# Kernel optimization log

Hardware: AMD Instinct MI355X
Metric: run time of the kernel (lower is better)

Reference implementation:

```python
import jax, jax.numpy as jnp
import numpy as np

B, T, V, E, H, C = 128, 512, 100000, 100, 128, 3


def _lstm_dir(xs, w_ih, w_hh, b, reverse=False):
    # xs: [T,B,D]; w_ih: [4H,D]; w_hh: [4H,H]; b: [4H] (b_ih+b_hh combined)
    Tn, Bn, _ = xs.shape
    Hn = w_hh.shape[1]
    if reverse:
        xs = xs[::-1]
    gx = jnp.einsum('tbd,gd->tbg', xs, w_ih) + b  # [T,B,4H] input projections

    def step(carry, g_in):
        h, c = carry
        gates = g_in + h @ w_hh.T
        i, f, g, o = jnp.split(gates, 4, axis=-1)  # torch gate order i,f,g,o
        i = jax.nn.sigmoid(i)
        f = jax.nn.sigmoid(f)
        g = jnp.tanh(g)
        o = jax.nn.sigmoid(o)
        c = f * c + i * g
        h = o * jnp.tanh(c)
        return (h, c), h

    init = (jnp.zeros((Bn, Hn), xs.dtype), jnp.zeros((Bn, Hn), xs.dtype))
    (h_last, _), hs = jax.lax.scan(step, init, gx)
    if reverse:
        hs = hs[::-1]
    return hs, h_last


def setup_inputs() -> dict:
    key = jax.random.key(0)
    ks = jax.random.split(key, 24)
    s_e = 1.0 / np.sqrt(H)

    def u(k, shape):
        return jax.random.uniform(k, shape, jnp.float32, -s_e, s_e)

    x = jax.random.randint(ks[0], (B, T), 0, V, dtype=jnp.int32)
    emb = jax.random.normal(ks[1], (V, E), jnp.float32)
    emb = emb.at[0].set(0.0)  # padding_idx=0
    inp = {'x': x, 'emb': emb}
    names = []
    idx = 2
    for layer, din in ((0, E), (1, 2 * H)):
        for suf in ('', 'r'):
            inp[f'w_ih_l{layer}{suf}'] = u(ks[idx], (4 * H, din)); idx += 1
            inp[f'w_hh_l{layer}{suf}'] = u(ks[idx], (4 * H, H)); idx += 1
            inp[f'b_ih_l{layer}{suf}'] = u(ks[idx], (4 * H,)); idx += 1
            inp[f'b_hh_l{layer}{suf}'] = u(ks[idx], (4 * H,)); idx += 1
    s_f = 1.0 / np.sqrt(2 * H)
    inp['fc_w'] = jax.random.uniform(ks[22], (C, 2 * H), jnp.float32, -s_f, s_f)
    inp['fc_b'] = jax.random.uniform(ks[23], (C,), jnp.float32, -s_f, s_f)
    return inp


def reference(x, emb, w_ih_l0, w_hh_l0, b_ih_l0, b_hh_l0,
              w_ih_l0r, w_hh_l0r, b_ih_l0r, b_hh_l0r,
              w_ih_l1, w_hh_l1, b_ih_l1, b_hh_l1,
              w_ih_l1r, w_hh_l1r, b_ih_l1r, b_hh_l1r,
              fc_w, fc_b):
    # dropout is identity in eval mode
    xe = emb[x]                      # [B,T,E]
    xs = jnp.transpose(xe, (1, 0, 2))  # [T,B,E]
    # layer 0 bidirectional
    hf0, _ = _lstm_dir(xs, w_ih_l0, w_hh_l0, b_ih_l0 + b_hh_l0, reverse=False)
    hb0, _ = _lstm_dir(xs, w_ih_l0r, w_hh_l0r, b_ih_l0r + b_hh_l0r, reverse=True)
    x1 = jnp.concatenate([hf0, hb0], axis=-1)  # [T,B,2H]
    # layer 1 bidirectional; only final hidden states needed
    _, hF = _lstm_dir(x1, w_ih_l1, w_hh_l1, b_ih_l1 + b_hh_l1, reverse=False)
    _, hB = _lstm_dir(x1, w_ih_l1r, w_hh_l1r, b_ih_l1r + b_hh_l1r, reverse=True)
    out = jnp.concatenate([hF, hB], axis=1)  # [B,2H] == cat(hidden[-2], hidden[-1])
    return out @ fc_w.T + fc_b  # [B,C]
```

## Files before the change

kernel.cpp:

```cpp
#include <hip/hip_runtime.h>
#include <hip/hip_bf16.h>
#include <math.h>

#define TT 512
#define BB 128
#define EE 100
#define HH 128
#define G4 512
#define K1 256

typedef __attribute__((ext_vector_type(8))) short bf16x8;
typedef __attribute__((ext_vector_type(4))) float f32x4;

__device__ inline unsigned short bf16_rne(float v) {
    __hip_bfloat16 h = __float2bfloat16(v);
    return *reinterpret_cast<unsigned short*>(&h);
}

__device__ inline void gload16(const void* g, void* l) {
    __builtin_amdgcn_global_load_lds(
        (const __attribute__((address_space(1))) void*)g,
        (__attribute__((address_space(3))) void*)l, 16, 0, 0);
}

template<int CTRL>
__device__ inline float dppf(float x) {
    int r = __builtin_amdgcn_update_dpp(0, __float_as_int(x), CTRL, 0xF, 0xF, true);
    return __int_as_float(r);
}

__global__ void embed_cvt(const int* __restrict__ x, const float* __restrict__ emb,
                          unsigned short* __restrict__ xs2) {
    int row = blockIdx.x;
    int k = threadIdx.x;
    int b = row & 127, t = row >> 7;
    int tok = x[b * TT + t];
    float v = (k < EE) ? emb[(size_t)tok * EE + k] : 0.f;
    xs2[(size_t)row * 128 + k] = bf16_rne(v);
}

__global__ void wcvt2(const float* __restrict__ srcf, const float* __restrict__ srcr,
                      int Kin, int Kp,
                      unsigned short* __restrict__ dstf, unsigned short* __restrict__ dstr) {
    const float* src = blockIdx.y ? srcr : srcf;
    unsigned short* dst = blockIdx.y ? dstr : dstf;
    int n = blockIdx.x;
    int k = threadIdx.x;
    int j = n & 3;
    int gate = ((j & 1) << 1) | (j >> 1);
    int r = gate * 128 + (n >> 2);
    float v = (k < Kin) ? src[(size_t)r * Kin + k] : 0.f;
    dst[(size_t)n * Kp + k] = bf16_rne(v);
}

__global__ void bias2(const float* __restrict__ bihf0, const float* __restrict__ bhhf0,
                      const float* __restrict__ bihr0, const float* __restrict__ bhhr0,
                      const float* __restrict__ bihf1, const float* __restrict__ bhhf1,
                      const float* __restrict__ bihr1, const float* __restrict__ bhhr1,
                      float* __restrict__ dst) {
    int n = blockIdx.x * 256 + threadIdx.x;
    int layer = n >> 10;
    int d = (n >> 9) & 1, m = n & 511;
    int j = m & 3;
    int gate = ((j & 1) << 1) | (j >> 1);
    int src = gate * 128 + (m >> 2);
    const float* a = layer ? (d ? bihr1 : bihf1) : (d ? bihr0 : bihf0);
    const float* c = layer ? (d ? bhhr1 : bhhf1) : (d ? bhhr0 : bhhf0);
    dst[n] = a[src] + c[src];
}

__global__ void whh_pack4(const float* __restrict__ w0f, const float* __restrict__ w0r,
                          const float* __restrict__ w1f, const float* __restrict__ w1r,
                          float* __restrict__ dstbase) {
    int which = blockIdx.y;
    const float* src = which == 0 ? w0f : which == 1 ? w0r : which == 2 ? w1f : w1r;
    float* dst = dstbase + (size_t)which * 128 * 128 * 4;
    int u = blockIdx.x;
    int k = threadIdx.x;
    float4 v;
    v.x = src[((size_t)(0 * 128 + u)) * 128 + k];
    v.y = src[((size_t)(1 * 128 + u)) * 128 + k];
    v.z = src[((size_t)(2 * 128 + u)) * 128 + k];
    v.w = src[((size_t)(3 * 128 + u)) * 128 + k];
    reinterpret_cast<float4*>(dst)[(size_t)u * 128 + k] = v;
}

template<int K2>
__global__ __launch_bounds__(256) void gemm_mfma(
    const unsigned short* __restrict__ A2,
    const unsigned short* __restrict__ W2cat,
    const float* __restrict__ biascat,
    float* __restrict__ Cf, float* __restrict__ Cr,
    int t_base)
{
    __shared__ bf16x8 As[1024];
    __shared__ bf16x8 Bs[1024];
    int tid = threadIdx.x;
    int s = blockIdx.y;
    int dir = blockIdx.x >> 2;
    int nBase = (blockIdx.x & 3) * 128;
    int t = dir ? (TT - 1 - t_base - s) : (t_base + s);
    float* C = dir ? Cr : Cf;
    const unsigned short* Abase = A2 + (size_t)t * BB * K2;
    const unsigned short* Wbase = W2cat + (size_t)(dir * 512 + nBase) * K2;
    int lane = tid & 63, wid = tid >> 6;
    int wr = wid >> 1, wc = wid & 1;
    int l15 = lane & 15, g = lane >> 4;

    f32x4 acc[4][4];
    const f32x4 z = {0.f, 0.f, 0.f, 0.f};
    #pragma unroll
    for (int i = 0; i < 4; ++i)
        #pragma unroll
        for (int j = 0; j < 4; ++j) acc[i][j] = z;

    for (int kt = 0; kt < K2 / 64; ++kt) {
        #pragma unroll
        for (int j = 0; j < 4; ++j) {
            int p = tid + j * 256;
            int row = p >> 3;
            int k16 = (p & 7) ^ (row & 7);
            size_t goff = (size_t)row * K2 + kt * 64 + k16 * 8;
            gload16(Abase + goff, &As[p]);
            gload16(Wbase + goff, &Bs[p]);
        }
        __syncthreads();
        #pragma unroll
        for (int ks = 0; ks < 2; ++ks) {
            bf16x8 af[4], bfr[4];
            #pragma unroll
            for (int i = 0; i < 4; ++i) {
                int arow = wr * 64 + i * 16 + l15;
                int abyte = arow * 128 + ((ks * 64 + g * 16) ^ ((arow & 7) << 4));
                af[i] = As[abyte >> 4];
                int brow = wc * 64 + i * 16 + l15;
                int bbyte = brow * 128 + ((ks * 64 + g * 16) ^ ((brow & 7) << 4));
                bfr[i] = Bs[bbyte >> 4];
            }
            #pragma unroll
            for (int i = 0; i < 4; ++i)
                #pragma unroll
                for (int j = 0; j < 4; ++j)
                    acc[i][j] = __builtin_amdgcn_mfma_f32_16x16x32_bf16(
                        af[i], bfr[j], acc[i][j], 0, 0, 0);
        }
        __syncthreads();
    }
    int l3 = l15 & 3;
    int cquad = l15 & 12;
    bool lb0 = (l15 & 1) != 0;
    bool lb1 = (l15 & 2) != 0;
    #pragma unroll
    for (int i = 0; i < 4; ++i) {
        int row = s * 128 + wr * 64 + i * 16 + g * 4 + l3;
        float* Crow = C + (size_t)row * G4;
        #pragma unroll
        for (int j = 0; j < 4; ++j) {
            int colb = nBase + wc * 64 + j * 16 + cquad;
            float4 bv = *reinterpret_cast<const float4*>(&biascat[dir * 512 + colb]);
            f32x4 v = acc[i][j];
            float t0 = dppf<0xB1>(v[1]);
            float t1 = dppf<0xB1>(v[0]);
            float t2 = dppf<0xB1>(v[3]);
            float t3 = dppf<0xB1>(v[2]);
            float T0 = lb0 ? t0 : v[0];
            float T1 = lb0 ? v[1] : t1;
            float T2 = lb0 ? t2 : v[2];
            float T3 = lb0 ? v[3] : t3;
            float s0 = dppf<0x4E>(T2);
            float s1 = dppf<0x4E>(T3);
            float s2 = dppf<0x4E>(T0);
            float s3 = dppf<0x4E>(T1);
            float W0 = lb1 ? s0 : T0;
            float W1 = lb1 ? s1 : T1;
            float W2 = lb1 ? T2 : s2;
            float W3 = lb1 ? T3 : s3;
            float4 outv = {W0 + bv.x, W1 + bv.y, W2 + bv.z, W3 + bv.w};
            *reinterpret_cast<float4*>(&Crow[colb]) = outv;
        }
    }
}

__device__ inline float sig_fast(float z) {
    return __builtin_amdgcn_rcpf(1.f + __expf(-z));
}

__global__ __launch_bounds__(512, 2) void lstm_chunk(
    const float* __restrict__ gxf,
    const float* __restrict__ gxr,
    const float* __restrict__ wpkf,
    const float* __restrict__ wpkr,
    float* __restrict__ h_state,
    float* __restrict__ c_state,
    unsigned short* __restrict__ out_x1,
    int t_base, int TC, int init)
{
    int blk = blockIdx.x;
    int dir = blk >> 7;
    int b   = blk & 127;
    const float* gx  = dir ? gxr : gxf;
    const float* wpk = dir ? wpkr : wpkf;
    int tid = threadIdx.x;
    int u = tid >> 2, q = tid & 3;

    const f32x4* wp4 = reinterpret_cast<const f32x4*>(wpk) + ((size_t)u * 128 + q * 32);
#define LW(i) const f32x4 w##i = wp4[i];
    LW(0)  LW(1)  LW(2)  LW(3)  LW(4)  LW(5)  LW(6)  LW(7)
    LW(8)  LW(9)  LW(10) LW(11) LW(12) LW(13) LW(14) LW(15)
    LW(16) LW(17) LW(18) LW(19) LW(20) LW(21) LW(22) LW(23)
    LW(24) LW(25) LW(26) LW(27) LW(28) LW(29) LW(30) LW(31)
#undef LW

    __shared__ float hb[2][160];
    int sbase = (dir * BB + b) * HH;
    int hslot = (u >> 5) * 40 + (u & 31);
    float c = init ? 0.f : c_state[sbase + u];
    float h = init ? 0.f : h_state[sbase + u];
    if (q == 0) hb[0][hslot] = h;
    __syncthreads();

    const float* gxrow = gx + b * G4 + tid;
    float gin = gxrow[0];
    bool odd2 = (q & 2) != 0;
    float fq = (q == 1) ? 2.f : 1.f;
    float bq = (q == 1) ? -1.f : 0.f;

    for (int s = 0; s < TC; ++s) {
        int p = s & 1;
        int sn = (s + 1 < TC) ? s + 1 : s;
        float gin_next = gxrow[(size_t)sn * BB * G4];

        const float4* hb4 = reinterpret_cast<const float4*>(&hb[p][40 * q]);
        float4 hv0 = hb4[0], hv1 = hb4[1], hv2 = hb4[2], hv3 = hb4[3];
        float4 hv4 = hb4[4], hv5 = hb4[5], hv6 = hb4[6], hv7 = hb4[7];

        f32x4 a0 = {0.f,0.f,0.f,0.f}, a1 = {0.f,0.f,0.f,0.f};
        f32x4 a2 = {0.f,0.f,0.f,0.f}, a3 = {0.f,0.f,0.f,0.f};
#define FM(i0,i1,i2,i3,HV) { \
        f32x4 hh; \
        hh = f32x4{HV.x,HV.x,HV.x,HV.x}; a0 = __builtin_elementwise_fma(w##i0, hh, a0); \
        hh = f32x4{HV.y,HV.y,HV.y,HV.y}; a1 = __builtin_elementwise_fma(w##i1, hh, a1); \
        hh = f32x4{HV.z,HV.z,HV.z,HV.z}; a2 = __builtin_elementwise_fma(w##i2, hh, a2); \
        hh = f32x4{HV.w,HV.w,HV.w,HV.w}; a3 = __builtin_elementwise_fma(w##i3, hh, a3); }
        FM(0,1,2,3,hv0)    FM(4,5,6,7,hv1)    FM(8,9,10,11,hv2)  FM(12,13,14,15,hv3)
        FM(16,17,18,19,hv4) FM(20,21,22,23,hv5) FM(24,25,26,27,hv6) FM(28,29,30,31,hv7)
#undef FM
        f32x4 acc = (a0 + a1) + (a2 + a3);

        float xs = acc.x + dppf<0xB1>(acc.x);
        float ys = acc.y + dppf<0xB1>(acc.y);
        float zs = acc.z + dppf<0xB1>(acc.z);
        float ws = acc.w + dppf<0xB1>(acc.w);
        bool oddq = (q & 1) != 0;
        float sa = oddq ? zs : xs;
        float sb = oddq ? ws : ys;
        float sa2 = sa + dppf<0x4E>(sa);
        float sb2 = sb + dppf<0x4E>(sb);
        float pre_dot = odd2 ? sb2 : sa2;

        float pre = pre_dot + gin;
        float act = __builtin_fmaf(sig_fast(pre * fq), fq, bq);

        float ig = dppf<0x00>(act);
        float gg = dppf<0x55>(act);
        float fg = dppf<0xAA>(act);
        float og = dppf<0xFF>(act);

        c = fg * c + ig * gg;
        float th = __builtin_fmaf(2.f, sig_fast(2.f * c), -1.f);
        h = og * th;

        if (q == 0) {
            hb[p ^ 1][hslot] = h;
            if (out_x1) {
                int tg = dir ? (TT - 1 - (t_base + s)) : (t_base + s);
                out_x1[((size_t)tg * BB + b) * 256 + dir * HH + u] = bf16_rne(h);
            }
        }
        asm volatile("s_waitcnt lgkmcnt(0)" ::: "memory");
        __builtin_amdgcn_s_barrier();
        asm volatile("" ::: "memory");
        gin = gin_next;
    }
    if (q == 0) {
        h_state[sbase + u] = h;
        c_state[sbase + u] = c;
    }
}

__global__ void fc_kernel(const float* __restrict__ h_state,
                          const float* __restrict__ fc_w,
                          const float* __restrict__ fc_b,
                          float* __restrict__ out) {
    int tid = blockIdx.x * blockDim.x + threadIdx.x;
    if (tid >= BB * 3) return;
    int b = tid / 3;
    int c = tid % 3;
    float acc = 0.f;
    for (int j = 0; j < 256; ++j) {
        float v = (j < HH) ? h_state[((size_t)0 * BB + b) * HH + j]
                           : h_state[((size_t)1 * BB + b) * HH + (j - HH)];
        acc += v * fc_w[c * 256 + j];
    }
    out[b * 3 + c] = acc + fc_b[c];
}

extern "C" void kernel_launch(void* const* d_in, const int* in_sizes, int n_in,
                              void* d_out, int out_size, void* d_ws, size_t ws_size,
                              hipStream_t stream) {
    const int*   x        = (const int*)  d_in[0];
    const float* emb      = (const float*)d_in[1];
    const float* w_ih_l0  = (const float*)d_in[2];
    const float* w_hh_l0  = (const float*)d_in[3];
    const float* b_ih_l0  = (const float*)d_in[4];
    const float* b_hh_l0  = (const float*)d_in[5];
    const float* w_ih_l0r = (const float*)d_in[6];
    const float* w_hh_l0r = (const float*)d_in[7];
    const float* b_ih_l0r = (const float*)d_in[8];
    const float* b_hh_l0r = (const float*)d_in[9];
    const float* w_ih_l1  = (const float*)d_in[10];
    const float* w_hh_l1  = (const float*)d_in[11];
    const float* b_ih_l1  = (const float*)d_in[12];
    const float* b_hh_l1  = (const float*)d_in[13];
    const float* w_ih_l1r = (const float*)d_in[14];
    const float* w_hh_l1r = (const float*)d_in[15];
    const float* b_ih_l1r = (const float*)d_in[16];
    const float* b_hh_l1r = (const float*)d_in[17];
    const float* fc_w     = (const float*)d_in[18];
    const float* fc_b     = (const float*)d_in[19];
    float* out = (float*)d_out;
    (void)in_sizes; (void)n_in; (void)out_size;

    size_t xs2_b   = (size_t)TT * BB * 128 * 2;
    size_t x1_b    = (size_t)TT * BB * 256 * 2;
    size_t w2l0_b  = (size_t)512 * 128 * 2;
    size_t w2l1_b  = (size_t)512 * 256 * 2;
    size_t bias_b  = (size_t)1024 * 4;
    size_t wpk_b   = (size_t)128 * 128 * 4 * 4;
    size_t state_b = (size_t)2 * BB * HH * 4;
    size_t fixed = xs2_b + x1_b + 2 * w2l0_b + 2 * w2l1_b + 2 * bias_b
                 + 4 * wpk_b + 2 * state_b + 4096;
    int TC = 512;
    while (TC > 8) {
        size_t chunk2 = (size_t)TC * BB * G4 * 4 * 2;
        if (fixed + chunk2 <= ws_size) break;
        TC >>= 1;
    }
    char* ws = (char*)d_ws;
    size_t off = 0;
    unsigned short* xs2   = (unsigned short*)(ws + off); off += xs2_b;
    unsigned short* x1_2  = (unsigned short*)(ws + off); off += x1_b;
    unsigned short* w2l0f = (unsigned short*)(ws + off); off += w2l0_b;
    unsigned short* w2l0r = (unsigned short*)(ws + off); off += w2l0_b;
    unsigned short* w2l1f = (unsigned short*)(ws + off); off += w2l1_b;
    unsigned short* w2l1r = (unsigned short*)(ws + off); off += w2l1_b;
    float* biasl0  = (float*)(ws + off); off += bias_b;
    float* biasl1  = (float*)(ws + off); off += bias_b;
    float* wpk0f   = (float*)(ws + off); off += wpk_b;
    float* wpk0r   = (float*)(ws + off); off += wpk_b;
    float* wpk1f   = (float*)(ws + off); off += wpk_b;
    float* wpk1r   = (float*)(ws + off); off += wpk_b;
    float* h_state = (float*)(ws + off); off += state_b;
    float* c_state = (float*)(ws + off); off += state_b;
    float* gxf     = (float*)(ws + off); off += (size_t)TC * BB * G4 * 4;
    float* gxr     = (float*)(ws + off);

    int NC = TT / TC;
    dim3 ggrid(8, TC);

    embed_cvt<<<TT * BB, 128, 0, stream>>>(x, emb, xs2);
    wcvt2<<<dim3(512, 2), 128, 0, stream>>>(w_ih_l0, w_ih_l0r, EE, 128, w2l0f, w2l0r);
    wcvt2<<<dim3(512, 2), 256, 0, stream>>>(w_ih_l1, w_ih_l1r, K1, 256, w2l1f, w2l1r);
    bias2<<<8, 256, 0, stream>>>(b_ih_l0, b_hh_l0, b_ih_l0r, b_hh_l0r,
                                 b_ih_l1, b_hh_l1, b_ih_l1r, b_hh_l1r, biasl0);
    whh_pack4<<<dim3(128, 4), 128, 0, stream>>>(w_hh_l0, w_hh_l0r, w_hh_l1, w_hh_l1r, wpk0f);

    for (int ci = 0; ci < NC; ++ci) {
        int t0 = ci * TC;
        gemm_mfma<128><<<ggrid, 256, 0, stream>>>(xs2, w2l0f, biasl0, gxf, gxr, t0);
        lstm_chunk<<<256, 512, 0, stream>>>(gxf, gxr, wpk0f, wpk0r,
                                            h_state, c_state, x1_2, t0, TC, ci == 0);
    }
    for (int ci = 0; ci < NC; ++ci) {
        int t0 = ci * TC;
        gemm_mfma<256><<<ggrid, 256, 0, stream>>>(x1_2, w2l1f, biasl1, gxf, gxr, t0);
        lstm_chunk<<<256, 512, 0, stream>>>(gxf, gxr, wpk1f, wpk1r,
                                            h_state, c_state, nullptr, t0, TC, ci == 0);
    }
    fc_kernel<<<2, 192, 0, stream>>>(h_state, fc_w, fc_b, out);
}
```

Before: 824.0 us.

## Fuse input-projection GEMM into recurrent LSTM kernel per chunk

Removes the separate MFMA GEMM kernel and its global gx buffer. Each recurrent block now computes its own batch row's input projections for 64-step chunks with MFMA, reading A and W straight from global memory, and keeps the result in ~130KB of shared memory. The recurrence then reads gates from LDS. This removes global round-trips and per-chunk launches, but the GEMM now runs serially inside each recurrent block. That loses the separate GEMM's tiling reuse, and the large LDS footprint limits occupancy to one block per CU.

```diff
diff --git a/kernel.cpp b/kernel.cpp
--- a/kernel.cpp
+++ b/kernel.cpp
@@ -17,16 +17,14 @@
     return *reinterpret_cast<unsigned short*>(&h);
 }
 
-__device__ inline void gload16(const void* g, void* l) {
-    __builtin_amdgcn_global_load_lds(
-        (const __attribute__((address_space(1))) void*)g,
-        (__attribute__((address_space(3))) void*)l, 16, 0, 0);
-}
-
 template<int CTRL>
 __device__ inline float dppf(float x) {
     int r = __builtin_amdgcn_update_dpp(0, __float_as_int(x), CTRL, 0xF, 0xF, true);
     return __int_as_float(r);
+}
+
+__device__ inline float sig_fast(float z) {
+    return __builtin_amdgcn_rcpf(1.f + __expf(-z));
 }
 
 __global__ void embed_cvt(const int* __restrict__ x, const float* __restrict__ emb,
@@ -86,122 +84,30 @@
 }
 
 template<int K2>
-__global__ __launch_bounds__(256) void gemm_mfma(
+__global__ __launch_bounds__(512, 1) void lstm_fused(
     const unsigned short* __restrict__ A2,
-    const unsigned short* __restrict__ W2cat,
+    const unsigned short* __restrict__ W2,
     const float* __restrict__ biascat,
-    float* __restrict__ Cf, float* __restrict__ Cr,
-    int t_base)
-{
-    __shared__ bf16x8 As[1024];
-    __shared__ bf16x8 Bs[1024];
-    int tid = threadIdx.x;
-    int s = blockIdx.y;
-    int dir = blockIdx.x >> 2;
-    int nBase = (blockIdx.x & 3) * 128;
-    int t = dir ? (TT - 1 - t_base - s) : (t_base + s);
-    float* C = dir ? Cr : Cf;
-    const unsigned short* Abase = A2 + (size_t)t * BB * K2;
-    const unsigned short* Wbase = W2cat + (size_t)(dir * 512 + nBase) * K2;
-    int lane = tid & 63, wid = tid >> 6;
-    int wr = wid >> 1, wc = wid & 1;
-    int l15 = lane & 15, g = lane >> 4;
-
-    f32x4 acc[4][4];
-    const f32x4 z = {0.f, 0.f, 0.f, 0.f};
-    #pragma unroll
-    for (int i = 0; i < 4; ++i)
-        #pragma unroll
-        for (int j = 0; j < 4; ++j) acc[i][j] = z;
-
-    for (int kt = 0; kt < K2 / 64; ++kt) {
-        #pragma unroll
-        for (int j = 0; j < 4; ++j) {
-            int p = tid + j * 256;
-            int row = p >> 3;
-            int k16 = (p & 7) ^ (row & 7);
-            size_t goff = (size_t)row * K2 + kt * 64 + k16 * 8;
-            gload16(Abase + goff, &As[p]);
-            gload16(Wbase + goff, &Bs[p]);
-        }
-        __syncthreads();
-        #pragma unroll
-        for (int ks = 0; ks < 2; ++ks) {
-            bf16x8 af[4], bfr[4];
-            #pragma unroll
-            for (int i = 0; i < 4; ++i) {
-                int arow = wr * 64 + i * 16 + l15;
-                int abyte = arow * 128 + ((ks * 64 + g * 16) ^ ((arow & 7) << 4));
-                af[i] = As[abyte >> 4];
-                int brow = wc * 64 + i * 16 + l15;
-                int bbyte = brow * 128 + ((ks * 64 + g * 16) ^ ((brow & 7) << 4));
-                bfr[i] = Bs[bbyte >> 4];
-            }
-            #pragma unroll
-            for (int i = 0; i < 4; ++i)
-                #pragma unroll
-                for (int j = 0; j < 4; ++j)
-                    acc[i][j] = __builtin_amdgcn_mfma_f32_16x16x32_bf16(
-                        af[i], bfr[j], acc[i][j], 0, 0, 0);
-        }
-        __syncthreads();
-    }
-    int l3 = l15 & 3;
-    int cquad = l15 & 12;
-    bool lb0 = (l15 & 1) != 0;
-    bool lb1 = (l15 & 2) != 0;
-    #pragma unroll
-    for (int i = 0; i < 4; ++i) {
-        int row = s * 128 + wr * 64 + i * 16 + g * 4 + l3;
-        float* Crow = C + (size_t)row * G4;
-        #pragma unroll
-        for (int j = 0; j < 4; ++j) {
-            int colb = nBase + wc * 64 + j * 16 + cquad;
-            float4 bv = *reinterpret_cast<const float4*>(&biascat[dir * 512 + colb]);
-            f32x4 v = acc[i][j];
-            float t0 = dppf<0xB1>(v[1]);
-            float t1 = dppf<0xB1>(v[0]);
-            float t2 = dppf<0xB1>(v[3]);
-            float t3 = dppf<0xB1>(v[2]);
-            float T0 = lb0 ? t0 : v[0];
-            float T1 = lb0 ? v[1] : t1;
-            float T2 = lb0 ? t2 : v[2];
-            float T3 = lb0 ? v[3] : t3;
-            float s0 = dppf<0x4E>(T2);
-            float s1 = dppf<0x4E>(T3);
-            float s2 = dppf<0x4E>(T0);
-            float s3 = dppf<0x4E>(T1);
-            float W0 = lb1 ? s0 : T0;
-            float W1 = lb1 ? s1 : T1;
-            float W2 = lb1 ? T2 : s2;
-            float W3 = lb1 ? T3 : s3;
-            float4 outv = {W0 + bv.x, W1 + bv.y, W2 + bv.z, W3 + bv.w};
-            *reinterpret_cast<float4*>(&Crow[colb]) = outv;
-        }
-    }
-}
-
-__device__ inline float sig_fast(float z) {
-    return __builtin_amdgcn_rcpf(1.f + __expf(-z));
-}
-
-__global__ __launch_bounds__(512, 2) void lstm_chunk(
-    const float* __restrict__ gxf,
-    const float* __restrict__ gxr,
     const float* __restrict__ wpkf,
     const float* __restrict__ wpkr,
-    float* __restrict__ h_state,
-    float* __restrict__ c_state,
     unsigned short* __restrict__ out_x1,
-    int t_base, int TC, int init)
+    float* __restrict__ hlast)
 {
+    constexpr int S = 64;
+    constexpr int NCH = TT / S;
+    constexpr int NKT = K2 / 32;
+
+    __shared__ float gxl[512 * 65];
+    __shared__ float hb[2][160];
+
     int blk = blockIdx.x;
     int dir = blk >> 7;
     int b   = blk & 127;
-    const float* gx  = dir ? gxr : gxf;
     const float* wpk = dir ? wpkr : wpkf;
     int tid = threadIdx.x;
     int u = tid >> 2, q = tid & 3;
+    int lane = tid & 63, w = tid >> 6;
+    int l15 = lane & 15, g = lane >> 4;
 
     const f32x4* wp4 = reinterpret_cast<const f32x4*>(wpk) + ((size_t)u * 128 + q * 32);
 #define LW(i) const f32x4 w##i = wp4[i];
@@ -211,81 +117,128 @@
     LW(24) LW(25) LW(26) LW(27) LW(28) LW(29) LW(30) LW(31)
 #undef LW
 
-    __shared__ float hb[2][160];
-    int sbase = (dir * BB + b) * HH;
+    const unsigned short* wbase[4];
+    float biasr[4];
+    #pragma unroll
+    for (int k = 0; k < 4; ++k) {
+        int n = (4 * w + k) * 16 + l15;
+        wbase[k] = W2 + (size_t)(dir * 512 + n) * K2 + g * 8;
+        biasr[k] = biascat[dir * 512 + n];
+    }
+
     int hslot = (u >> 5) * 40 + (u & 31);
-    float c = init ? 0.f : c_state[sbase + u];
-    float h = init ? 0.f : h_state[sbase + u];
-    if (q == 0) hb[0][hslot] = h;
-    __syncthreads();
-
-    const float* gxrow = gx + b * G4 + tid;
-    float gin = gxrow[0];
+    float h = 0.f, c = 0.f;
+    if (q == 0) hb[0][hslot] = 0.f;
+
     bool odd2 = (q & 2) != 0;
+    bool oddq = (q & 1) != 0;
     float fq = (q == 1) ? 2.f : 1.f;
     float bq = (q == 1) ? -1.f : 0.f;
-
-    for (int s = 0; s < TC; ++s) {
-        int p = s & 1;
-        int sn = (s + 1 < TC) ? s + 1 : s;
-        float gin_next = gxrow[(size_t)sn * BB * G4];
-
-        const float4* hb4 = reinterpret_cast<const float4*>(&hb[p][40 * q]);
-        float4 hv0 = hb4[0], hv1 = hb4[1], hv2 = hb4[2], hv3 = hb4[3];
-        float4 hv4 = hb4[4], hv5 = hb4[5], hv6 = hb4[6], hv7 = hb4[7];
-
-        f32x4 a0 = {0.f,0.f,0.f,0.f}, a1 = {0.f,0.f,0.f,0.f};
-        f32x4 a2 = {0.f,0.f,0.f,0.f}, a3 = {0.f,0.f,0.f,0.f};
+    float* gxrow = &gxl[tid * 65];
+
+    for (int ch = 0; ch < NCH; ++ch) {
+        __syncthreads();
+        const unsigned short* abase[4];
+        #pragma unroll
+        for (int m = 0; m < 4; ++m) {
+            int sg = ch * S + m * 16 + l15;
+            int t = dir ? (TT - 1 - sg) : sg;
+            abase[m] = A2 + ((size_t)t * BB + b) * K2 + g * 8;
+        }
+        #pragma unroll
+        for (int p = 0; p < 2; ++p) {
+            f32x4 acc[4][2];
+            const f32x4 z = {0.f, 0.f, 0.f, 0.f};
+            #pragma unroll
+            for (int m = 0; m < 4; ++m) {
+                acc[m][0] = z; acc[m][1] = z;
+            }
+            #pragma unroll
+            for (int kt = 0; kt < NKT; ++kt) {
+                bf16x8 af[4], bfr[2];
+                #pragma unroll
+                for (int m = 0; m < 4; ++m)
+                    af[m] = *reinterpret_cast<const bf16x8*>(abase[m] + kt * 32);
+                #pragma unroll
+                for (int jj = 0; jj < 2; ++jj)
+                    bfr[jj] = *reinterpret_cast<const bf16x8*>(wbase[2 * p + jj] + kt * 32);
+                #pragma unroll
+                for (int m = 0; m < 4; ++m)
+                    #pragma unroll
+                    for (int jj = 0; jj < 2; ++jj)
+                        acc[m][jj] = __builtin_amdgcn_mfma_f32_16x16x32_bf16(
+                            af[m], bfr[jj], acc[m][jj], 0, 0, 0);
+            }
+            #pragma unroll
+            for (int m = 0; m < 4; ++m)
+                #pragma unroll
+                for (int jj = 0; jj < 2; ++jj) {
+                    int col = (4 * w + 2 * p + jj) * 16 + l15;
+                    int s0 = m * 16 + g * 4;
+                    float bv = biasr[2 * p + jj];
+                    #pragma unroll
+                    for (int r = 0; r < 4; ++r)
+                        gxl[col * 65 + s0 + r] = acc[m][jj][r] + bv;
+                }
+        }
+        __syncthreads();
+        for (int sl = 0; sl < S; ++sl) {
+            int p2 = sl & 1;
+            float gin = gxrow[sl];
+
+            const float4* hb4 = reinterpret_cast<const float4*>(&hb[p2][40 * q]);
+            float4 hv0 = hb4[0], hv1 = hb4[1], hv2 = hb4[2], hv3 = hb4[3];
+            float4 hv4 = hb4[4], hv5 = hb4[5], hv6 = hb4[6], hv7 = hb4[7];
+
+            f32x4 a0 = {0.f,0.f,0.f,0.f}, a1 = {0.f,0.f,0.f,0.f};
+            f32x4 a2 = {0.f,0.f,0.f,0.f}, a3 = {0.f,0.f,0.f,0.f};
 #define FM(i0,i1,i2,i3,HV) { \
-        f32x4 hh; \
-        hh = f32x4{HV.x,HV.x,HV.x,HV.x}; a0 = __builtin_elementwise_fma(w##i0, hh, a0); \
-        hh = f32x4{HV.y,HV.y,HV.y,HV.y}; a1 = __builtin_elementwise_fma(w##i1, hh, a1); \
-        hh = f32x4{HV.z,HV.z,HV.z,HV.z}; a2 = __builtin_elementwise_fma(w##i2, hh, a2); \
-        hh = f32x4{HV.w,HV.w,HV.w,HV.w}; a3 = __builtin_elementwise_fma(w##i3, hh, a3); }
-        FM(0,1,2,3,hv0)    FM(4,5,6,7,hv1)    FM(8,9,10,11,hv2)  FM(12,13,14,15,hv3)
-        FM(16,17,18,19,hv4) FM(20,21,22,23,hv5) FM(24,25,26,27,hv6) FM(28,29,30,31,hv7)
+            f32x4 hh; \
+            hh = f32x4{HV.x,HV.x,HV.x,HV.x}; a0 = __builtin_elementwise_fma(w##i0, hh, a0); \
+            hh = f32x4{HV.y,HV.y,HV.y,HV.y}; a1 = __builtin_elementwise_fma(w##i1, hh, a1); \
+            hh = f32x4{HV.z,HV.z,HV.z,HV.z}; a2 = __builtin_elementwise_fma(w##i2, hh, a2); \
+            hh = f32x4{HV.w,HV.w,HV.w,HV.w}; a3 = __builtin_elementwise_fma(w##i3, hh, a3); }
+            FM(0,1,2,3,hv0)     FM(4,5,6,7,hv1)     FM(8,9,10,11,hv2)   FM(12,13,14,15,hv3)
+            FM(16,17,18,19,hv4) FM(20,21,22,23,hv5) FM(24,25,26,27,hv6) FM(28,29,30,31,hv7)
 #undef FM
-        f32x4 acc = (a0 + a1) + (a2 + a3);
-
-        float xs = acc.x + dppf<0xB1>(acc.x);
-        float ys = acc.y + dppf<0xB1>(acc.y);
-        float zs = acc.z + dppf<0xB1>(acc.z);
-        float ws = acc.w + dppf<0xB1>(acc.w);
-        bool oddq = (q & 1) != 0;
-        float sa = oddq ? zs : xs;
-        float sb = oddq ? ws : ys;
-        float sa2 = sa + dppf<0x4E>(sa);
-        float sb2 = sb + dppf<0x4E>(sb);
-        float pre_dot = odd2 ? sb2 : sa2;
-
-        float pre = pre_dot + gin;
-        float act = __builtin_fmaf(sig_fast(pre * fq), fq, bq);
-
-        float ig = dppf<0x00>(act);
-        float gg = dppf<0x55>(act);
-        float fg = dppf<0xAA>(act);
-        float og = dppf<0xFF>(act);
-
-        c = fg * c + ig * gg;
-        float th = __builtin_fmaf(2.f, sig_fast(2.f * c), -1.f);
-        h = og * th;
-
-        if (q == 0) {
-            hb[p ^ 1][hslot] = h;
-            if (out_x1) {
-                int tg = dir ? (TT - 1 - (t_base + s)) : (t_base + s);
-                out_x1[((size_t)tg * BB + b) * 256 + dir * HH + u] = bf16_rne(h);
+            f32x4 acc = (a0 + a1) + (a2 + a3);
+
+            float xs = acc.x + dppf<0xB1>(acc.x);
+            float ys = acc.y + dppf<0xB1>(acc.y);
+            float zs = acc.z + dppf<0xB1>(acc.z);
+            float ws = acc.w + dppf<0xB1>(acc.w);
+            float sa = oddq ? zs : xs;
+            float sb = oddq ? ws : ys;
+            float sa2 = sa + dppf<0x4E>(sa);
+            float sb2 = sb + dppf<0x4E>(sb);
+            float pre_dot = odd2 ? sb2 : sa2;
+
+            float pre = pre_dot + gin;
+            float act = __builtin_fmaf(sig_fast(pre * fq), fq, bq);
+
+            float ig = dppf<0x00>(act);
+            float gg = dppf<0x55>(act);
+            float fg = dppf<0xAA>(act);
+            float og = dppf<0xFF>(act);
+
+            c = fg * c + ig * gg;
+            float th = __builtin_fmaf(2.f, sig_fast(2.f * c), -1.f);
+            h = og * th;
+
+            if (q == 0) {
+                hb[p2 ^ 1][hslot] = h;
+                if (out_x1) {
+                    int tg = dir ? (TT - 1 - (ch * S + sl)) : (ch * S + sl);
+                    out_x1[((size_t)tg * BB + b) * 256 + dir * HH + u] = bf16_rne(h);
+                }
             }
+            asm volatile("s_waitcnt lgkmcnt(0)" ::: "memory");
+            __builtin_amdgcn_s_barrier();
+            asm volatile("" ::: "memory");
         }
-        asm volatile("s_waitcnt lgkmcnt(0)" ::: "memory");
-        __builtin_amdgcn_s_barrier();
-        asm volatile("" ::: "memory");
-        gin = gin_next;
     }
-    if (q == 0) {
-        h_state[sbase + u] = h;
-        c_state[sbase + u] = c;
-    }
+    if (hlast && q == 0)
+        hlast[(dir * BB + b) * HH + u] = h;
 }
 
 __global__ void fc_kernel(const float* __restrict__ h_state,
@@ -329,7 +282,7 @@
     const float* fc_w     = (const float*)d_in[18];
     const float* fc_b     = (const float*)d_in[19];
     float* out = (float*)d_out;
-    (void)in_sizes; (void)n_in; (void)out_size;
+    (void)in_sizes; (void)n_in; (void)out_size; (void)ws_size;
 
     size_t xs2_b   = (size_t)TT * BB * 128 * 2;
     size_t x1_b    = (size_t)TT * BB * 256 * 2;
@@ -338,14 +291,6 @@
     size_t bias_b  = (size_t)1024 * 4;
     size_t wpk_b   = (size_t)128 * 128 * 4 * 4;
     size_t state_b = (size_t)2 * BB * HH * 4;
-    size_t fixed = xs2_b + x1_b + 2 * w2l0_b + 2 * w2l1_b + 2 * bias_b
-                 + 4 * wpk_b + 2 * state_b + 4096;
-    int TC = 512;
-    while (TC > 8) {
-        size_t chunk2 = (size_t)TC * BB * G4 * 4 * 2;
-        if (fixed + chunk2 <= ws_size) break;
-        TC >>= 1;
-    }
     char* ws = (char*)d_ws;
     size_t off = 0;
     unsigned short* xs2   = (unsigned short*)(ws + off); off += xs2_b;
@@ -361,12 +306,6 @@
     float* wpk1f   = (float*)(ws + off); off += wpk_b;
     float* wpk1r   = (float*)(ws + off); off += wpk_b;
     float* h_state = (float*)(ws + off); off += state_b;
-    float* c_state = (float*)(ws + off); off += state_b;
-    float* gxf     = (float*)(ws + off); off += (size_t)TC * BB * G4 * 4;
-    float* gxr     = (float*)(ws + off);
-
-    int NC = TT / TC;
-    dim3 ggrid(8, TC);
 
     embed_cvt<<<TT * BB, 128, 0, stream>>>(x, emb, xs2);
     wcvt2<<<dim3(512, 2), 128, 0, stream>>>(w_ih_l0, w_ih_l0r, EE, 128, w2l0f, w2l0r);
@@ -375,17 +314,9 @@
                                  b_ih_l1, b_hh_l1, b_ih_l1r, b_hh_l1r, biasl0);
     whh_pack4<<<dim3(128, 4), 128, 0, stream>>>(w_hh_l0, w_hh_l0r, w_hh_l1, w_hh_l1r, wpk0f);
 
-    for (int ci = 0; ci < NC; ++ci) {
-        int t0 = ci * TC;
-        gemm_mfma<128><<<ggrid, 256, 0, stream>>>(xs2, w2l0f, biasl0, gxf, gxr, t0);
-        lstm_chunk<<<256, 512, 0, stream>>>(gxf, gxr, wpk0f, wpk0r,
-                                            h_state, c_state, x1_2, t0, TC, ci == 0);
-    }
-    for (int ci = 0; ci < NC; ++ci) {
-        int t0 = ci * TC;
-        gemm_mfma<256><<<ggrid, 256, 0, stream>>>(x1_2, w2l1f, biasl1, gxf, gxr, t0);
-        lstm_chunk<<<256, 512, 0, stream>>>(gxf, gxr, wpk1f, wpk1r,
-                                            h_state, c_state, nullptr, t0, TC, ci == 0);
-    }
+    lstm_fused<128><<<256, 512, 0, stream>>>(xs2, w2l0f, biasl0, wpk0f, wpk0r,
+                                             x1_2, nullptr);
+    lstm_fused<256><<<256, 512, 0, stream>>>(x1_2, w2l1f, biasl1, wpk1f, wpk1r,
+                                             nullptr, h_state);
     fc_kernel<<<2, 192, 0, stream>>>(h_state, fc_w, fc_b, out);
 }
```

New measurement: 870.5 us. +5.6%, slower.

## Fuse layer-0 input projection GEMM into the recurrent LSTM kernel

Applied to the files above, without the earlier changes.

Adds a fused kernel for layer 0 in which each block (one batch row, one direction) computes its input-gate projections with MFMA into LDS, chunk by chunk, and then runs the recurrence over that chunk. This removes the global round-trip of the fp32 gx buffer and the separate GEMM launches for layer 0. Each block now redoes the projection with the W_ih fragments held in registers, at the cost of higher register and LDS pressure and one block per CU. Layer 1 keeps the separate GEMM plus recurrence path, and its chunk size cap drops to 256 steps.

```diff
diff --git a/kernel.cpp b/kernel.cpp
--- a/kernel.cpp
+++ b/kernel.cpp
@@ -27,6 +27,10 @@
 __device__ inline float dppf(float x) {
     int r = __builtin_amdgcn_update_dpp(0, __float_as_int(x), CTRL, 0xF, 0xF, true);
     return __int_as_float(r);
+}
+
+__device__ inline float sig_fast(float z) {
+    return __builtin_amdgcn_rcpf(1.f + __expf(-z));
 }
 
 __global__ void embed_cvt(const int* __restrict__ x, const float* __restrict__ emb,
@@ -83,6 +87,164 @@
     v.z = src[((size_t)(2 * 128 + u)) * 128 + k];
     v.w = src[((size_t)(3 * 128 + u)) * 128 + k];
     reinterpret_cast<float4*>(dst)[(size_t)u * 128 + k] = v;
+}
+
+template<int K2, int S, int STRIDE>
+__global__ __launch_bounds__(512, 1) void lstm_fused(
+    const unsigned short* __restrict__ A2,
+    const unsigned short* __restrict__ W2,
+    const float* __restrict__ biascat,
+    const float* __restrict__ wpkf,
+    const float* __restrict__ wpkr,
+    unsigned short* __restrict__ out_x1,
+    float* __restrict__ hlast)
+{
+    constexpr int NCH = TT / S;
+    constexpr int NKT = K2 / 32;
+    constexpr int CPR = K2 / 8;
+    constexpr int M   = S / 16;
+
+    __shared__ float gxl[512 * STRIDE];
+    __shared__ bf16x8 Asl[1024];
+    __shared__ float hb[2][160];
+
+    int blk = blockIdx.x;
+    int dir = blk >> 7;
+    int b   = blk & 127;
+    const float* wpk = dir ? wpkr : wpkf;
+    int tid = threadIdx.x;
+    int u = tid >> 2, q = tid & 3;
+    int lane = tid & 63, w = tid >> 6;
+    int l15 = lane & 15, g = lane >> 4;
+
+    const f32x4* wp4 = reinterpret_cast<const f32x4*>(wpk) + ((size_t)u * 128 + q * 32);
+#define LW(i) const f32x4 w##i = wp4[i];
+    LW(0)  LW(1)  LW(2)  LW(3)  LW(4)  LW(5)  LW(6)  LW(7)
+    LW(8)  LW(9)  LW(10) LW(11) LW(12) LW(13) LW(14) LW(15)
+    LW(16) LW(17) LW(18) LW(19) LW(20) LW(21) LW(22) LW(23)
+    LW(24) LW(25) LW(26) LW(27) LW(28) LW(29) LW(30) LW(31)
+#undef LW
+
+    bf16x8 wf[NKT][4];
+    float biasr[4];
+    #pragma unroll
+    for (int cg = 0; cg < 4; ++cg) {
+        int n = (4 * w + cg) * 16 + l15;
+        const unsigned short* wb = W2 + (size_t)(dir * 512 + n) * K2 + g * 8;
+        biasr[cg] = biascat[dir * 512 + n];
+        #pragma unroll
+        for (int kt = 0; kt < NKT; ++kt)
+            wf[kt][cg] = *reinterpret_cast<const bf16x8*>(wb + kt * 32);
+    }
+
+    int hslot = (u >> 5) * 40 + (u & 31);
+    float h = 0.f, c = 0.f;
+    if (q == 0) hb[0][hslot] = 0.f;
+
+    bool odd2 = (q & 2) != 0;
+    bool oddq = (q & 1) != 0;
+    float fq = (q == 1) ? 2.f : 1.f;
+    float bq = (q == 1) ? -1.f : 0.f;
+    float* gxrow = &gxl[tid * STRIDE];
+
+    for (int ch = 0; ch < NCH; ++ch) {
+        __syncthreads();
+        #pragma unroll
+        for (int j = 0; j < 2; ++j) {
+            int slot = tid + j * 512;
+            int row = slot / CPR;
+            int cl = slot % CPR;
+            int cs = cl ^ (row & 7);
+            int sg = ch * S + row;
+            int t = dir ? (TT - 1 - sg) : sg;
+            gload16(A2 + ((size_t)t * BB + b) * K2 + cs * 8, &Asl[slot]);
+        }
+        __syncthreads();
+        #pragma unroll
+        for (int cg = 0; cg < 4; ++cg) {
+            f32x4 acc4[M];
+            const f32x4 z = {0.f, 0.f, 0.f, 0.f};
+            #pragma unroll
+            for (int m = 0; m < M; ++m) acc4[m] = z;
+            #pragma unroll
+            for (int kt = 0; kt < NKT; ++kt) {
+                #pragma unroll
+                for (int m = 0; m < M; ++m) {
+                    int row = m * 16 + l15;
+                    int cc = (kt * 4 + g) ^ (row & 7);
+                    bf16x8 af = Asl[row * CPR + cc];
+                    acc4[m] = __builtin_amdgcn_mfma_f32_16x16x32_bf16(
+                        af, wf[kt][cg], acc4[m], 0, 0, 0);
+                }
+            }
+            int col = (4 * w + cg) * 16 + l15;
+            float bv = biasr[cg];
+            #pragma unroll
+            for (int m = 0; m < M; ++m) {
+                int s0 = m * 16 + g * 4;
+                #pragma unroll
+                for (int r = 0; r < 4; ++r)
+                    gxl[col * STRIDE + s0 + r] = acc4[m][r] + bv;
+            }
+        }
+        __syncthreads();
+        for (int sl = 0; sl < S; ++sl) {
+            int p2 = sl & 1;
+            float gin = gxrow[sl];
+
+            const float4* hb4 = reinterpret_cast<const float4*>(&hb[p2][40 * q]);
+            float4 hv0 = hb4[0], hv1 = hb4[1], hv2 = hb4[2], hv3 = hb4[3];
+            float4 hv4 = hb4[4], hv5 = hb4[5], hv6 = hb4[6], hv7 = hb4[7];
+
+            f32x4 a0 = {0.f,0.f,0.f,0.f}, a1 = {0.f,0.f,0.f,0.f};
+            f32x4 a2 = {0.f,0.f,0.f,0.f}, a3 = {0.f,0.f,0.f,0.f};
+#define FM(i0,i1,i2,i3,HV) { \
+            f32x4 hh; \
+            hh = f32x4{HV.x,HV.x,HV.x,HV.x}; a0 = __builtin_elementwise_fma(w##i0, hh, a0); \
+            hh = f32x4{HV.y,HV.y,HV.y,HV.y}; a1 = __builtin_elementwise_fma(w##i1, hh, a1); \
+            hh = f32x4{HV.z,HV.z,HV.z,HV.z}; a2 = __builtin_elementwise_fma(w##i2, hh, a2); \
+            hh = f32x4{HV.w,HV.w,HV.w,HV.w}; a3 = __builtin_elementwise_fma(w##i3, hh, a3); }
+            FM(0,1,2,3,hv0)     FM(4,5,6,7,hv1)     FM(8,9,10,11,hv2)   FM(12,13,14,15,hv3)
+            FM(16,17,18,19,hv4) FM(20,21,22,23,hv5) FM(24,25,26,27,hv6) FM(28,29,30,31,hv7)
+#undef FM
+            f32x4 acc = (a0 + a1) + (a2 + a3);
+
+            float xs = acc.x + dppf<0xB1>(acc.x);
+            float ys = acc.y + dppf<0xB1>(acc.y);
+            float zs = acc.z + dppf<0xB1>(acc.z);
+            float ws = acc.w + dppf<0xB1>(acc.w);
+            float sa = oddq ? zs : xs;
+            float sb = oddq ? ws : ys;
+            float sa2 = sa + dppf<0x4E>(sa);
+            float sb2 = sb + dppf<0x4E>(sb);
+            float pre_dot = odd2 ? sb2 : sa2;
+
+            float pre = pre_dot + gin;
+            float act = __builtin_fmaf(sig_fast(pre * fq), fq, bq);
+
+            float ig = dppf<0x00>(act);
+            float gg = dppf<0x55>(act);
+            float fg = dppf<0xAA>(act);
+            float og = dppf<0xFF>(act);
+
+            c = fg * c + ig * gg;
+            float th = __builtin_fmaf(2.f, sig_fast(2.f * c), -1.f);
+            h = og * th;
+
+            if (q == 0) {
+                hb[p2 ^ 1][hslot] = h;
+                if (out_x1) {
+                    int tg = dir ? (TT - 1 - (ch * S + sl)) : (ch * S + sl);
+                    out_x1[((size_t)tg * BB + b) * 256 + dir * HH + u] = bf16_rne(h);
+                }
+            }
+            asm volatile("s_waitcnt lgkmcnt(0)" ::: "memory");
+            __builtin_amdgcn_s_barrier();
+            asm volatile("" ::: "memory");
+        }
+    }
+    if (hlast && q == 0)
+        hlast[(dir * BB + b) * HH + u] = h;
 }
 
 template<int K2>
@@ -179,10 +341,6 @@
             *reinterpret_cast<float4*>(&Crow[colb]) = outv;
         }
     }
-}
-
-__device__ inline float sig_fast(float z) {
-    return __builtin_amdgcn_rcpf(1.f + __expf(-z));
 }
 
 __global__ __launch_bounds__(512, 2) void lstm_chunk(
@@ -340,7 +498,7 @@
     size_t state_b = (size_t)2 * BB * HH * 4;
     size_t fixed = xs2_b + x1_b + 2 * w2l0_b + 2 * w2l1_b + 2 * bias_b
                  + 4 * wpk_b + 2 * state_b + 4096;
-    int TC = 512;
+    int TC = 256;
     while (TC > 8) {
         size_t chunk2 = (size_t)TC * BB * G4 * 4 * 2;
         if (fixed + chunk2 <= ws_size) break;
@@ -366,7 +524,6 @@
     float* gxr     = (float*)(ws + off);
 
     int NC = TT / TC;
-    dim3 ggrid(8, TC);
 
     embed_cvt<<<TT * BB, 128, 0, stream>>>(x, emb, xs2);
     wcvt2<<<dim3(512, 2), 128, 0, stream>>>(w_ih_l0, w_ih_l0r, EE, 128, w2l0f, w2l0r);
@@ -375,15 +532,11 @@
                                  b_ih_l1, b_hh_l1, b_ih_l1r, b_hh_l1r, biasl0);
     whh_pack4<<<dim3(128, 4), 128, 0, stream>>>(w_hh_l0, w_hh_l0r, w_hh_l1, w_hh_l1r, wpk0f);
 
+    lstm_fused<128, 64, 65><<<256, 512, 0, stream>>>(xs2, w2l0f, biasl0, wpk0f, wpk0r,
+                                                     x1_2, nullptr);
     for (int ci = 0; ci < NC; ++ci) {
         int t0 = ci * TC;
-        gemm_mfma<128><<<ggrid, 256, 0, stream>>>(xs2, w2l0f, biasl0, gxf, gxr, t0);
-        lstm_chunk<<<256, 512, 0, stream>>>(gxf, gxr, wpk0f, wpk0r,
-                                            h_state, c_state, x1_2, t0, TC, ci == 0);
-    }
-    for (int ci = 0; ci < NC; ++ci) {
-        int t0 = ci * TC;
-        gemm_mfma<256><<<ggrid, 256, 0, stream>>>(x1_2, w2l1f, biasl1, gxf, gxr, t0);
+        gemm_mfma<256><<<dim3(8, TC), 256, 0, stream>>>(x1_2, w2l1f, biasl1, gxf, gxr, t0);
         lstm_chunk<<<256, 512, 0, stream>>>(gxf, gxr, wpk1f, wpk1r,
                                             h_state, c_state, nullptr, t0, TC, ci == 0);
     }
```

Result: faster. 790.5 us (-4.1%).
